# Performance work log

Measured on AMD Instinct MI355X. Metric: run time of the kernel, lower is better.

## Reference

```python
import jax, jax.numpy as jnp
import numpy as np

INF = 100000.0
B, W, T, U, S, N = 64, 16, 64, 128, 20, 8


def setup_inputs() -> dict:
    key = jax.random.key(0)
    ks = jax.random.split(key, 9)
    xavier = (2.0 / (U + U)) ** 0.5
    return {
        "slot_utt_h": jax.random.normal(ks[0], (B, W, T, U), jnp.float32),
        "slot_candidate_c": jax.random.normal(ks[1], (S, U), jnp.float32),
        "status_candidate_c": jax.random.normal(ks[2], (N, U), jnp.float32),
        "position_encoding": jax.random.normal(ks[3], (B, W, S, U), jnp.float32),
        "q_status": jax.random.normal(ks[4], (B, W, N, U), jnp.float32),
        "mask": jnp.zeros((B, W, S * N), jnp.float32),
        "weight": jax.random.normal(ks[5], (U, U), jnp.float32) * xavier,  # bilinear co-attention weight [U,U]
        "W1": jax.random.normal(ks[6], (2 * U, U), jnp.float32) * 0.05,
        "b1": jnp.zeros((U,), jnp.float32),
        "W2": jax.random.normal(ks[7], (U, U), jnp.float32) * 0.05,
        "b2": jnp.zeros((U,), jnp.float32),
        "W3": jax.random.normal(ks[8], (U, 1), jnp.float32) * 0.05,
        "b3": jnp.zeros((1,), jnp.float32),
    }


def _zero_mask(p):
    # original: -(p == 0).float() * INF, added before softmax
    return jnp.where(p == 0.0, -INF, 0.0)


def reference(slot_utt_h, slot_candidate_c, status_candidate_c, position_encoding,
              q_status, mask, weight, W1, b1, W2, b2, W3, b3):
    # ---- attention over utterance tokens ----
    # p[b,w,s,t] = <slot_candidate_c[s], slot_utt_h[b,w,t]>
    p = jnp.einsum('su,bwtu->bwst', slot_candidate_c, slot_utt_h)
    p = jax.nn.softmax(p + _zero_mask(p), axis=-1)
    q_slot = jnp.einsum('bwst,bwtu->bwsu', p, slot_utt_h) + position_encoding  # [B,W,S,U]

    # ---- bilinear co-attention: [B,W*S,U] @ weight @ [B,U,W*N] -> [B,W,S,W,N] ----
    co = jnp.einsum('bwsu,uv,bxnv->bwsxn', q_slot, weight, q_status)
    p2 = jax.nn.softmax(co + _zero_mask(co), axis=3)  # softmax over the second window axis x

    # weighted sum of statuses over window axis x
    q_status_slot = jnp.einsum('bwsxn,bxnu->bwsnu', p2, q_status)  # [B,W,S,N,U]

    q_slot_exp = jnp.broadcast_to(q_slot[:, :, :, None, :], (B, W, S, N, U))
    features = jnp.concatenate([q_slot_exp, q_status_slot], axis=-1)  # [B,W,S,N,2U]

    # ---- MLP (dropout in eval mode = identity) ----
    h = jax.nn.relu(features @ W1 + b1)
    h = jax.nn.relu(h @ W2 + b2)
    logits = h @ W3 + b3  # [B,W,S,N,1]

    logits = logits.reshape(B, W, S * N)
    slot_pred_logits = jnp.max(logits + mask, axis=1)  # masked max-pool over window
    slot_pred_labels = (slot_pred_logits > 0.0).astype(jnp.float32)
    return (slot_pred_labels, S * N, slot_pred_logits)
```

## Files before the change

### kernel.cpp

```cpp
#include <hip/hip_runtime.h>
#include <math.h>

#define INF_ 100000.0f
constexpr int B_ = 64, W_ = 16, T_ = 64, U_ = 128, S_ = 20, N_ = 8;

typedef unsigned short ushort_t;
typedef __attribute__((ext_vector_type(8))) short bf16x8;
typedef __attribute__((ext_vector_type(4))) float floatx4;

static __device__ __forceinline__ unsigned short f2bf(float x) {
    unsigned int u = __float_as_uint(x);
    return (unsigned short)((u + 0x7fff + ((u >> 16) & 1)) >> 16);
}
static __device__ __forceinline__ float bf2f(unsigned short s) {
    return __uint_as_float(((unsigned int)s) << 16);
}

#define HT_SWZ(u, t) ((u) * 72 + ((t) ^ ((((u) >> 3) & 7) << 3)))

__global__ __launch_bounds__(256) void kAP(
    const float* __restrict__ q_status, const float* __restrict__ weight,
    const float* __restrict__ W1, const float* __restrict__ W2,
    const float* __restrict__ c,
    const float* __restrict__ h,
    const float* __restrict__ pos,
    ushort_t* __restrict__ w1topT, ushort_t* __restrict__ w2T,
    ushort_t* __restrict__ Gt_bf, ushort_t* __restrict__ qs1T_bf,
    ushort_t* __restrict__ q_slot_bf)
{
    __shared__ __align__(16) ushort_t arena[17408];
    const int tid = threadIdx.x, bx = blockIdx.x;
    const int wave = tid >> 6, lane = tid & 63, m16 = lane & 15, q = lane >> 4;
    const bf16x8 zz = {0, 0, 0, 0, 0, 0, 0, 0};

    if (bx < 64) {
        const int b = bx;
        for (int i = tid * 4; i < 16384; i += 1024) {
            int r = i >> 7, v = i & 127;
            float4 wv = *(const float4*)&weight[i];
            *(ushort4*)&arena[r * 136 + v] =
                (ushort4){f2bf(wv.x), f2bf(wv.y), f2bf(wv.z), f2bf(wv.w)};
        }
        __syncthreads();
        const float* qb = q_status + (size_t)b * 16384;
        ushort_t* Gb = Gt_bf + (size_t)b * 16384;
#pragma unroll
        for (int mt2 = 0; mt2 < 2; ++mt2) {
            int mt = wave * 2 + mt2;
            int arow = mt * 16 + m16;
            bf16x8 afr[4];
#pragma unroll
            for (int kt = 0; kt < 4; ++kt) {
                const float* qp = &qb[arow * 128 + kt * 32 + q * 8];
                float4 c0 = *(const float4*)&qp[0];
                float4 c1 = *(const float4*)&qp[4];
                bf16x8 a;
                a[0] = (short)f2bf(c0.x); a[1] = (short)f2bf(c0.y);
                a[2] = (short)f2bf(c0.z); a[3] = (short)f2bf(c0.w);
                a[4] = (short)f2bf(c1.x); a[5] = (short)f2bf(c1.y);
                a[6] = (short)f2bf(c1.z); a[7] = (short)f2bf(c1.w);
                afr[kt] = a;
            }
#pragma unroll
            for (int jt = 0; jt < 8; ++jt) {
                floatx4 acc = {0.f, 0.f, 0.f, 0.f};
#pragma unroll
                for (int kt = 0; kt < 4; ++kt) {
                    bf16x8 w = *(const bf16x8*)&arena[(jt * 16 + m16) * 136 + kt * 32 + q * 8];
                    acc = __builtin_amdgcn_mfma_f32_16x16x32_bf16(afr[kt], w, acc, 0, 0, 0);
                }
#pragma unroll
                for (int reg = 0; reg < 4; ++reg)
                    Gb[(mt * 16 + q * 4 + reg) * 128 + jt * 16 + m16] = f2bf(acc[reg]);
            }
        }
        return;
    }
    if (bx < 128) {
        const int b = bx - 64;
        for (int i = tid * 4; i < 16384; i += 1024) {
            int v2 = i >> 7, j = i & 127;
            float4 wv = *(const float4*)&W1[(128 + v2) * 128 + j];
            arena[(j + 0) * 136 + v2] = f2bf(wv.x);
            arena[(j + 1) * 136 + v2] = f2bf(wv.y);
            arena[(j + 2) * 136 + v2] = f2bf(wv.z);
            arena[(j + 3) * 136 + v2] = f2bf(wv.w);
        }
        __syncthreads();
        const float* qb = q_status + (size_t)b * 16384;
        ushort_t* Qb = qs1T_bf + (size_t)b * 16384;
#pragma unroll
        for (int mt2 = 0; mt2 < 2; ++mt2) {
            int mt = wave * 2 + mt2;
            int arow = mt * 16 + m16;
            bf16x8 afr[4];
#pragma unroll
            for (int kt = 0; kt < 4; ++kt) {
                const float* qp = &qb[arow * 128 + kt * 32 + q * 8];
                float4 c0 = *(const float4*)&qp[0];
                float4 c1 = *(const float4*)&qp[4];
                bf16x8 a;
                a[0] = (short)f2bf(c0.x); a[1] = (short)f2bf(c0.y);
                a[2] = (short)f2bf(c0.z); a[3] = (short)f2bf(c0.w);
                a[4] = (short)f2bf(c1.x); a[5] = (short)f2bf(c1.y);
                a[6] = (short)f2bf(c1.z); a[7] = (short)f2bf(c1.w);
                afr[kt] = a;
            }
#pragma unroll
            for (int jt = 0; jt < 8; ++jt) {
                floatx4 acc = {0.f, 0.f, 0.f, 0.f};
#pragma unroll
                for (int kt = 0; kt < 4; ++kt) {
                    bf16x8 w = *(const bf16x8*)&arena[(jt * 16 + m16) * 136 + kt * 32 + q * 8];
                    acc = __builtin_amdgcn_mfma_f32_16x16x32_bf16(afr[kt], w, acc, 0, 0, 0);
                }
                ushort4 o = {f2bf(acc[0]), f2bf(acc[1]), f2bf(acc[2]), f2bf(acc[3])};
                *(ushort4*)&Qb[(jt * 16 + m16) * 128 + mt * 16 + q * 4] = o;
            }
        }
        return;
    }
    if (bx < 144) {
        int g = (bx - 128) * 1024 + tid * 4;
        int j = g >> 7, k = g & 127;
        *(ushort4*)&w1topT[g] =
            (ushort4){f2bf(W1[k * 128 + j]), f2bf(W1[(k + 1) * 128 + j]),
                      f2bf(W1[(k + 2) * 128 + j]), f2bf(W1[(k + 3) * 128 + j])};
        return;
    }
    if (bx < 160) {
        int g = (bx - 144) * 1024 + tid * 4;
        int j = g >> 7, k = g & 127;
        *(ushort4*)&w2T[g] =
            (ushort4){f2bf(W2[k * 128 + j]), f2bf(W2[(k + 1) * 128 + j]),
                      f2bf(W2[(k + 2) * 128 + j]), f2bf(W2[(k + 3) * 128 + j])};
        return;
    }

    ushort_t* sh_hT = arena;
    float*    sh_sc = (float*)(arena + 9216);
    ushort_t* sh_P  = arena + 13568;

    const int bw = bx - 160;
    const float* hb = h + (size_t)bw * 8192;

    for (int i = tid * 4; i < 8192; i += 1024) {
        int t = i >> 7, u = i & 127;
        float4 v = *(const float4*)&hb[i];
        sh_hT[HT_SWZ(u + 0, t)] = f2bf(v.x);
        sh_hT[HT_SWZ(u + 1, t)] = f2bf(v.y);
        sh_hT[HT_SWZ(u + 2, t)] = f2bf(v.z);
        sh_hT[HT_SWZ(u + 3, t)] = f2bf(v.w);
    }
    for (int i = tid; i < 2304; i += 256) sh_P[i] = 0;

#pragma unroll
    for (int ci = 0; ci < 2; ++ci) {
        int cmb = wave * 2 + ci;
        int mt = cmb >> 2, jt = cmb & 3;
        int arow = mt * 16 + m16;
        floatx4 acc = {0.f, 0.f, 0.f, 0.f};
#pragma unroll
        for (int kt = 0; kt < 4; ++kt) {
            bf16x8 a = zz;
            if (arow < 20) {
                const float* cp = &c[arow * 128 + kt * 32 + q * 8];
                float4 c0 = *(const float4*)&cp[0];
                float4 c1 = *(const float4*)&cp[4];
                a[0] = (short)f2bf(c0.x); a[1] = (short)f2bf(c0.y);
                a[2] = (short)f2bf(c0.z); a[3] = (short)f2bf(c0.w);
                a[4] = (short)f2bf(c1.x); a[5] = (short)f2bf(c1.y);
                a[6] = (short)f2bf(c1.z); a[7] = (short)f2bf(c1.w);
            }
            const float* hp = &hb[(jt * 16 + m16) * 128 + kt * 32 + q * 8];
            float4 b0 = *(const float4*)&hp[0];
            float4 b1v = *(const float4*)&hp[4];
            bf16x8 bb;
            bb[0] = (short)f2bf(b0.x); bb[1] = (short)f2bf(b0.y);
            bb[2] = (short)f2bf(b0.z); bb[3] = (short)f2bf(b0.w);
            bb[4] = (short)f2bf(b1v.x); bb[5] = (short)f2bf(b1v.y);
            bb[6] = (short)f2bf(b1v.z); bb[7] = (short)f2bf(b1v.w);
            acc = __builtin_amdgcn_mfma_f32_16x16x32_bf16(a, bb, acc, 0, 0, 0);
        }
#pragma unroll
        for (int reg = 0; reg < 4; ++reg)
            sh_sc[(mt * 16 + q * 4 + reg) * 68 + jt * 16 + m16] = acc[reg];
    }
    __syncthreads();

    for (int s = wave; s < 20; s += 4) {
        float v = sh_sc[s * 68 + lane];
        if (v == 0.0f) v = -INF_;
        float m = v;
        for (int d = 32; d; d >>= 1) m = fmaxf(m, __shfl_xor(m, d));
        float e = expf(v - m);
        float sum = e;
        for (int d = 32; d; d >>= 1) sum += __shfl_xor(sum, d);
        sh_P[s * 72 + lane] = f2bf(e / sum);
    }
    __syncthreads();

    const size_t obase = (size_t)bw * 2560;
#pragma unroll
    for (int ci = 0; ci < 4; ++ci) {
        int cmb = wave * 4 + ci;
        int mt = cmb >> 3, jt = cmb & 7;
        floatx4 acc = {0.f, 0.f, 0.f, 0.f};
#pragma unroll
        for (int kt = 0; kt < 2; ++kt) {
            bf16x8 a = *(const bf16x8*)&sh_P[(mt * 16 + m16) * 72 + kt * 32 + q * 8];
            bf16x8 b = *(const bf16x8*)&sh_hT[HT_SWZ(jt * 16 + m16, kt * 32 + q * 8)];
            acc = __builtin_amdgcn_mfma_f32_16x16x32_bf16(a, b, acc, 0, 0, 0);
        }
        int u = jt * 16 + m16;
#pragma unroll
        for (int reg = 0; reg < 4; ++reg) {
            int row = mt * 16 + q * 4 + reg;
            if (row < 20)
                q_slot_bf[obase + row * 128 + u] =
                    f2bf(acc[reg] + pos[obase + row * 128 + u]);
        }
    }
}

__global__ __launch_bounds__(640, 8) void kCp(
    const ushort_t* __restrict__ q_slot_bf,
    const ushort_t* __restrict__ Gt_bf,
    const ushort_t* __restrict__ w1topT,
    const float* __restrict__ b1,
    const ushort_t* __restrict__ qs1T_bf,
    const ushort_t* __restrict__ w2T,
    const float* __restrict__ b2,
    const float* __restrict__ W3,
    const float* __restrict__ b3,
    float* __restrict__ lg)
{
    __shared__ __align__(16) ushort_t arena[25328];
    float* Af = (float*)(arena + 20048);

    const int bw = blockIdx.x, b = bw >> 4, tid = threadIdx.x;
    const int wave = tid >> 6, lane = tid & 63, m16 = lane & 15, q = lane >> 4;
    const bf16x8 zz = {0, 0, 0, 0, 0, 0, 0, 0};

    for (int i = tid * 4; i < 16384; i += 2560) {
        int r = i >> 7, k = i & 127;
        *(ushort4*)&arena[r * 136 + k] = *(const ushort4*)&qs1T_bf[(size_t)b * 16384 + i];
    }
    {
        const ushort_t* qsl = q_slot_bf + (size_t)bw * 2560;
        const ushort_t* Gb = Gt_bf + (size_t)b * 16384;
        for (int t = wave; t < 32; t += 10) {
            int isA = t >> 4, tt = t & 15;
            int mt = tt >> 3, jt = tt & 7;
            int arow = mt * 16 + m16;
            const ushort_t* Bsrc = isA ? w1topT : Gb;
            floatx4 acc = {0.f, 0.f, 0.f, 0.f};
#pragma unroll
            for (int kt = 0; kt < 4; ++kt) {
                bf16x8 a = (arow < 20)
                    ? *(const bf16x8*)&qsl[arow * 128 + kt * 32 + q * 8] : zz;
                bf16x8 g = *(const bf16x8*)&Bsrc[(jt * 16 + m16) * 128 + kt * 32 + q * 8];
                acc = __builtin_amdgcn_mfma_f32_16x16x32_bf16(a, g, acc, 0, 0, 0);
            }
            int col = jt * 16 + m16;
            if (isA) {
                float bv = b1[col];
#pragma unroll
                for (int reg = 0; reg < 4; ++reg) {
                    int row = mt * 16 + q * 4 + reg;
                    if (row < 20) Af[row * 132 + col] = acc[reg] + bv;
                }
            } else {
#pragma unroll
                for (int reg = 0; reg < 4; ++reg) {
                    int row = mt * 16 + q * 4 + reg;
                    if (row < 20) arena[17408 + row * 132 + col] = f2bf(acc[reg]);
                }
            }
        }
    }
    __syncthreads();

    {
        int sn = tid >> 2, xi = tid & 3;
        int s = sn >> 3, n2 = sn & 7;
        const ushort_t* crow = &arena[17408 + s * 132];
        float v[4];
        float m = -INFINITY;
#pragma unroll
        for (int j = 0; j < 4; ++j) {
            float t = bf2f(crow[(xi + 4 * j) * 8 + n2]);
            if (t == 0.0f) t = -INF_;
            v[j] = t;
            m = fmaxf(m, t);
        }
        m = fmaxf(m, __shfl_xor(m, 1));
        m = fmaxf(m, __shfl_xor(m, 2));
        float sum = 0.f;
#pragma unroll
        for (int j = 0; j < 4; ++j) { v[j] = expf(v[j] - m); sum += v[j]; }
        sum += __shfl_xor(sum, 1);
        sum += __shfl_xor(sum, 2);
        float r = 1.0f / sum;
        __syncthreads();
#pragma unroll
        for (int j = 0; j < 4; ++j)
            arena[17408 + s * 132 + (xi + 4 * j) * 8 + n2] = f2bf(v[j] * r);
    }
    __syncthreads();

    const int n = m16 & 7;
    const int sIdx = wave * 2 + (m16 >> 3);

    floatx4 gacc[8];
#pragma unroll
    for (int mt = 0; mt < 8; ++mt) gacc[mt] = (floatx4){0.f, 0.f, 0.f, 0.f};
#pragma unroll
    for (int kt = 0; kt < 4; ++kt) {
        short pv = (short)arena[17408 + sIdx * 132 + kt * 32 + q * 8 + n];
        bf16x8 pf = {0, 0, 0, 0, 0, 0, 0, 0};
        pf[0] = (n == 0) ? pv : (short)0;
        pf[1] = (n == 1) ? pv : (short)0;
        pf[2] = (n == 2) ? pv : (short)0;
        pf[3] = (n == 3) ? pv : (short)0;
        pf[4] = (n == 4) ? pv : (short)0;
        pf[5] = (n == 5) ? pv : (short)0;
        pf[6] = (n == 6) ? pv : (short)0;
        pf[7] = (n == 7) ? pv : (short)0;
#pragma unroll
        for (int mt = 0; mt < 8; ++mt) {
            bf16x8 af = *(const bf16x8*)&arena[(mt * 16 + m16) * 136 + kt * 32 + q * 8];
            gacc[mt] = __builtin_amdgcn_mfma_f32_16x16x32_bf16(af, pf, gacc[mt], 0, 0, 0);
        }
    }

    unsigned int h1u[8][2];
    {
        const float* Ab = Af + sIdx * 132;
#pragma unroll
        for (int mt = 0; mt < 8; ++mt) {
            int u0 = mt * 16 + q * 4;
            float4 av = *(const float4*)&Ab[u0];
            unsigned int x0 = f2bf(fmaxf(gacc[mt][0] + av.x, 0.f));
            unsigned int x1 = f2bf(fmaxf(gacc[mt][1] + av.y, 0.f));
            unsigned int x2 = f2bf(fmaxf(gacc[mt][2] + av.z, 0.f));
            unsigned int x3 = f2bf(fmaxf(gacc[mt][3] + av.w, 0.f));
            h1u[mt][0] = x0 | (x1 << 16);
            h1u[mt][1] = x2 | (x3 << 16);
        }
    }
    __syncthreads();

    for (int i = tid * 4; i < 16384; i += 2560) {
        int r = i >> 7, k = i & 127;
        *(ushort4*)&arena[r * 136 + k] = *(const ushort4*)&w2T[i];
    }
    __syncthreads();

    floatx4 acc[8];
#pragma unroll
    for (int jt = 0; jt < 8; ++jt) acc[jt] = (floatx4){0.f, 0.f, 0.f, 0.f};

    const int sl0 = m16 + 16 * ((2 * q) & 3);
    const int sl1 = m16 + 16 * ((2 * q + 1) & 3);
    const bool hi = (q & 2);
#pragma unroll
    for (int kt = 0; kt < 4; ++kt) {
        int wa0 = __shfl((int)h1u[kt * 2 + 0][0], sl0);
        int wb0 = __shfl((int)h1u[kt * 2 + 1][0], sl0);
        int wa1 = __shfl((int)h1u[kt * 2 + 0][1], sl0);
        int wb1 = __shfl((int)h1u[kt * 2 + 1][1], sl0);
        int wa2 = __shfl((int)h1u[kt * 2 + 0][0], sl1);
        int wb2 = __shfl((int)h1u[kt * 2 + 1][0], sl1);
        int wa3 = __shfl((int)h1u[kt * 2 + 0][1], sl1);
        int wb3 = __shfl((int)h1u[kt * 2 + 1][1], sl1);
        int4 fr;
        fr.x = hi ? wb0 : wa0;
        fr.y = hi ? wb1 : wa1;
        fr.z = hi ? wb2 : wa2;
        fr.w = hi ? wb3 : wa3;
        bf16x8 af2 = *(bf16x8*)&fr;
        const int k0 = kt * 32 + q * 8;
#pragma unroll
        for (int jt = 0; jt < 8; ++jt) {
            bf16x8 bfr = *(const bf16x8*)&arena[(jt * 16 + m16) * 136 + k0];
            acc[jt] = __builtin_amdgcn_mfma_f32_16x16x32_bf16(af2, bfr, acc[jt], 0, 0, 0);
        }
    }

    float b2v[8], w3v[8];
#pragma unroll
    for (int jt = 0; jt < 8; ++jt) {
        b2v[jt] = b2[jt * 16 + m16];
        w3v[jt] = W3[jt * 16 + m16];
    }
    const float b3v = b3[0];
#pragma unroll
    for (int reg = 0; reg < 4; ++reg) {
        float p = 0.f;
#pragma unroll
        for (int jt = 0; jt < 8; ++jt)
            p += fmaxf(acc[jt][reg] + b2v[jt], 0.f) * w3v[jt];
        p += __shfl_xor(p, 1);
        p += __shfl_xor(p, 2);
        p += __shfl_xor(p, 4);
        p += __shfl_xor(p, 8);
        if (m16 == 0)
            lg[(size_t)bw * 160 + wave * 16 + q * 4 + reg] = p + b3v;
    }
}

__global__ __launch_bounds__(256) void k5_final(
    const float* __restrict__ lg,
    const float* __restrict__ mask,
    float* __restrict__ out)
{
    int idx = blockIdx.x * 256 + threadIdx.x;
    const int SN = S_ * N_;
    if (idx < B_ * SN) {
        int b = idx / SN, sn = idx % SN;
        float m = -INFINITY;
        for (int w = 0; w < W_; ++w) {
            float v = lg[((size_t)b * W_ + w) * SN + sn] + mask[((size_t)b * W_ + w) * SN + sn];
            m = fmaxf(m, v);
        }
        out[idx] = (m > 0.f) ? 1.f : 0.f;
        out[B_ * SN + 1 + idx] = m;
    }
    if (idx == 0) out[B_ * SN] = (float)SN;
}

extern "C" void kernel_launch(void* const* d_in, const int* in_sizes, int n_in,
                              void* d_out, int out_size, void* d_ws, size_t ws_size,
                              hipStream_t stream) {
    const float* slot_utt_h = (const float*)d_in[0];
    const float* slot_candidate_c = (const float*)d_in[1];
    const float* position_encoding = (const float*)d_in[3];
    const float* q_status = (const float*)d_in[4];
    const float* mask = (const float*)d_in[5];
    const float* weight = (const float*)d_in[6];
    const float* W1 = (const float*)d_in[7];
    const float* b1 = (const float*)d_in[8];
    const float* W2 = (const float*)d_in[9];
    const float* b2 = (const float*)d_in[10];
    const float* W3 = (const float*)d_in[11];
    const float* b3 = (const float*)d_in[12];
    float* out = (float*)d_out;

    float* f = (float*)d_ws;
    float*    lg        = f + 0;
    ushort_t* q_slot_bf = (ushort_t*)(f + 163840);
    ushort_t* Gt_bf     = (ushort_t*)(f + 1474560);
    ushort_t* qs1T_bf   = (ushort_t*)(f + 1998848);
    ushort_t* w1topT    = (ushort_t*)(f + 2523136);
    ushort_t* w2T       = (ushort_t*)(f + 2531328);

    kAP<<<1184, 256, 0, stream>>>(q_status, weight, W1, W2,
                                  slot_candidate_c, slot_utt_h,
                                  position_encoding,
                                  w1topT, w2T, Gt_bf, qs1T_bf, q_slot_bf);
    kCp<<<1024, 640, 0, stream>>>(q_slot_bf, Gt_bf, w1topT, b1, qs1T_bf,
                                  w2T, b2, W3, b3, lg);
    k5_final<<<(B_ * S_ * N_ + 255) / 256, 256, 0, stream>>>(lg, mask, out);
}
```

Baseline: 186.2 us.

## Split co-attention and W1 projection GEMMs into a separate batched kernel

Moves the q_slot x G co-attention product and the q_slot x W1top projection out of the per-(b,w) kernel into a new kernel. That kernel stages the B operand in shared memory and computes 64-row tiles across windows, so each block reuses G or W1top far more than the old 20-row blocks, which read B straight from global memory. The results (co in bf16, A in fp32) now round-trip through global workspace, adding an extra launch and extra memory traffic, and the remaining kernel's occupancy hint changes from 8 to 5.

```diff
diff --git a/kernel.cpp b/kernel.cpp
--- a/kernel.cpp
+++ b/kernel.cpp
@@ -223,68 +223,99 @@
     }
 }
 
-__global__ __launch_bounds__(640, 8) void kCp(
+__global__ __launch_bounds__(256) void kB(
     const ushort_t* __restrict__ q_slot_bf,
     const ushort_t* __restrict__ Gt_bf,
     const ushort_t* __restrict__ w1topT,
     const float* __restrict__ b1,
+    ushort_t* __restrict__ co_bf,
+    float* __restrict__ A)
+{
+    __shared__ __align__(16) ushort_t shB[128 * 136];
+    const int tid = threadIdx.x, bx = blockIdx.x;
+    const int wave = tid >> 6, lane = tid & 63, m16 = lane & 15, q = lane >> 4;
+
+    if (bx < 320) {
+        const int b = bx / 5, rt = bx - b * 5;
+        for (int i = tid * 4; i < 16384; i += 1024)
+            *(ushort4*)&shB[(i >> 7) * 136 + (i & 127)] =
+                *(const ushort4*)&Gt_bf[(size_t)b * 16384 + i];
+        __syncthreads();
+
+        const size_t rbase = (size_t)b * 320 + rt * 64 + wave * 16;
+        floatx4 acc[8];
+#pragma unroll
+        for (int jt = 0; jt < 8; ++jt) acc[jt] = (floatx4){0.f, 0.f, 0.f, 0.f};
+#pragma unroll
+        for (int kt = 0; kt < 4; ++kt) {
+            bf16x8 a = *(const bf16x8*)&q_slot_bf[(rbase + m16) * 128 + kt * 32 + q * 8];
+#pragma unroll
+            for (int jt = 0; jt < 8; ++jt) {
+                bf16x8 g = *(const bf16x8*)&shB[(jt * 16 + m16) * 136 + kt * 32 + q * 8];
+                acc[jt] = __builtin_amdgcn_mfma_f32_16x16x32_bf16(a, g, acc[jt], 0, 0, 0);
+            }
+        }
+#pragma unroll
+        for (int jt = 0; jt < 8; ++jt)
+#pragma unroll
+            for (int reg = 0; reg < 4; ++reg)
+                co_bf[(rbase + q * 4 + reg) * 128 + jt * 16 + m16] = f2bf(acc[jt][reg]);
+    } else {
+        const int blk = bx - 320;
+        for (int i = tid * 4; i < 16384; i += 1024)
+            *(ushort4*)&shB[(i >> 7) * 136 + (i & 127)] =
+                *(const ushort4*)&w1topT[i];
+        __syncthreads();
+
+        const size_t rbase = (size_t)blk * 64 + wave * 16;
+        floatx4 acc[8];
+#pragma unroll
+        for (int jt = 0; jt < 8; ++jt) acc[jt] = (floatx4){0.f, 0.f, 0.f, 0.f};
+#pragma unroll
+        for (int kt = 0; kt < 4; ++kt) {
+            bf16x8 a = *(const bf16x8*)&q_slot_bf[(rbase + m16) * 128 + kt * 32 + q * 8];
+#pragma unroll
+            for (int jt = 0; jt < 8; ++jt) {
+                bf16x8 g = *(const bf16x8*)&shB[(jt * 16 + m16) * 136 + kt * 32 + q * 8];
+                acc[jt] = __builtin_amdgcn_mfma_f32_16x16x32_bf16(a, g, acc[jt], 0, 0, 0);
+            }
+        }
+#pragma unroll
+        for (int jt = 0; jt < 8; ++jt) {
+            int col = jt * 16 + m16;
+            float bv = b1[col];
+#pragma unroll
+            for (int reg = 0; reg < 4; ++reg)
+                A[(rbase + q * 4 + reg) * 128 + col] = acc[jt][reg] + bv;
+        }
+    }
+}
+
+__global__ __launch_bounds__(640, 5) void kC(
+    const ushort_t* __restrict__ co_bf,
     const ushort_t* __restrict__ qs1T_bf,
+    const float* __restrict__ A,
     const ushort_t* __restrict__ w2T,
     const float* __restrict__ b2,
     const float* __restrict__ W3,
     const float* __restrict__ b3,
     float* __restrict__ lg)
 {
-    __shared__ __align__(16) ushort_t arena[25328];
-    float* Af = (float*)(arena + 20048);
+    __shared__ __align__(16) ushort_t shB[128 * 136];
+    __shared__ __align__(16) ushort_t shP[20 * 132];
 
     const int bw = blockIdx.x, b = bw >> 4, tid = threadIdx.x;
     const int wave = tid >> 6, lane = tid & 63, m16 = lane & 15, q = lane >> 4;
-    const bf16x8 zz = {0, 0, 0, 0, 0, 0, 0, 0};
 
     for (int i = tid * 4; i < 16384; i += 2560) {
         int r = i >> 7, k = i & 127;
-        *(ushort4*)&arena[r * 136 + k] = *(const ushort4*)&qs1T_bf[(size_t)b * 16384 + i];
-    }
-    {
-        const ushort_t* qsl = q_slot_bf + (size_t)bw * 2560;
-        const ushort_t* Gb = Gt_bf + (size_t)b * 16384;
-        for (int t = wave; t < 32; t += 10) {
-            int isA = t >> 4, tt = t & 15;
-            int mt = tt >> 3, jt = tt & 7;
-            int arow = mt * 16 + m16;
-            const ushort_t* Bsrc = isA ? w1topT : Gb;
-            floatx4 acc = {0.f, 0.f, 0.f, 0.f};
-#pragma unroll
-            for (int kt = 0; kt < 4; ++kt) {
-                bf16x8 a = (arow < 20)
-                    ? *(const bf16x8*)&qsl[arow * 128 + kt * 32 + q * 8] : zz;
-                bf16x8 g = *(const bf16x8*)&Bsrc[(jt * 16 + m16) * 128 + kt * 32 + q * 8];
-                acc = __builtin_amdgcn_mfma_f32_16x16x32_bf16(a, g, acc, 0, 0, 0);
-            }
-            int col = jt * 16 + m16;
-            if (isA) {
-                float bv = b1[col];
-#pragma unroll
-                for (int reg = 0; reg < 4; ++reg) {
-                    int row = mt * 16 + q * 4 + reg;
-                    if (row < 20) Af[row * 132 + col] = acc[reg] + bv;
-                }
-            } else {
-#pragma unroll
-                for (int reg = 0; reg < 4; ++reg) {
-                    int row = mt * 16 + q * 4 + reg;
-                    if (row < 20) arena[17408 + row * 132 + col] = f2bf(acc[reg]);
-                }
-            }
-        }
-    }
-    __syncthreads();
+        *(ushort4*)&shB[r * 136 + k] = *(const ushort4*)&qs1T_bf[(size_t)b * 16384 + i];
+    }
 
     {
         int sn = tid >> 2, xi = tid & 3;
         int s = sn >> 3, n2 = sn & 7;
-        const ushort_t* crow = &arena[17408 + s * 132];
+        const ushort_t* crow = co_bf + ((size_t)bw * 20 + s) * 128;
         float v[4];
         float m = -INFINITY;
 #pragma unroll
@@ -302,10 +333,9 @@
         sum += __shfl_xor(sum, 1);
         sum += __shfl_xor(sum, 2);
         float r = 1.0f / sum;
-        __syncthreads();
 #pragma unroll
         for (int j = 0; j < 4; ++j)
-            arena[17408 + s * 132 + (xi + 4 * j) * 8 + n2] = f2bf(v[j] * r);
+            shP[s * 132 + (xi + 4 * j) * 8 + n2] = f2bf(v[j] * r);
     }
     __syncthreads();
 
@@ -317,7 +347,7 @@
     for (int mt = 0; mt < 8; ++mt) gacc[mt] = (floatx4){0.f, 0.f, 0.f, 0.f};
 #pragma unroll
     for (int kt = 0; kt < 4; ++kt) {
-        short pv = (short)arena[17408 + sIdx * 132 + kt * 32 + q * 8 + n];
+        short pv = (short)shP[sIdx * 132 + kt * 32 + q * 8 + n];
         bf16x8 pf = {0, 0, 0, 0, 0, 0, 0, 0};
         pf[0] = (n == 0) ? pv : (short)0;
         pf[1] = (n == 1) ? pv : (short)0;
@@ -329,14 +359,14 @@
         pf[7] = (n == 7) ? pv : (short)0;
 #pragma unroll
         for (int mt = 0; mt < 8; ++mt) {
-            bf16x8 af = *(const bf16x8*)&arena[(mt * 16 + m16) * 136 + kt * 32 + q * 8];
+            bf16x8 af = *(const bf16x8*)&shB[(mt * 16 + m16) * 136 + kt * 32 + q * 8];
             gacc[mt] = __builtin_amdgcn_mfma_f32_16x16x32_bf16(af, pf, gacc[mt], 0, 0, 0);
         }
     }
 
     unsigned int h1u[8][2];
     {
-        const float* Ab = Af + sIdx * 132;
+        const float* Ab = A + ((size_t)bw * 20 + sIdx) * 128;
 #pragma unroll
         for (int mt = 0; mt < 8; ++mt) {
             int u0 = mt * 16 + q * 4;
@@ -353,7 +383,7 @@
 
     for (int i = tid * 4; i < 16384; i += 2560) {
         int r = i >> 7, k = i & 127;
-        *(ushort4*)&arena[r * 136 + k] = *(const ushort4*)&w2T[i];
+        *(ushort4*)&shB[r * 136 + k] = *(const ushort4*)&w2T[i];
     }
     __syncthreads();
 
@@ -383,7 +413,7 @@
         const int k0 = kt * 32 + q * 8;
 #pragma unroll
         for (int jt = 0; jt < 8; ++jt) {
-            bf16x8 bfr = *(const bf16x8*)&arena[(jt * 16 + m16) * 136 + k0];
+            bf16x8 bfr = *(const bf16x8*)&shB[(jt * 16 + m16) * 136 + k0];
             acc[jt] = __builtin_amdgcn_mfma_f32_16x16x32_bf16(af2, bfr, acc[jt], 0, 0, 0);
         }
     }
@@ -449,17 +479,19 @@
 
     float* f = (float*)d_ws;
     float*    lg        = f + 0;
-    ushort_t* q_slot_bf = (ushort_t*)(f + 163840);
-    ushort_t* Gt_bf     = (ushort_t*)(f + 1474560);
-    ushort_t* qs1T_bf   = (ushort_t*)(f + 1998848);
-    ushort_t* w1topT    = (ushort_t*)(f + 2523136);
-    ushort_t* w2T       = (ushort_t*)(f + 2531328);
+    float*    A         = f + 163840;
+    ushort_t* q_slot_bf = (ushort_t*)(f + 2785280);
+    ushort_t* co_bf     = (ushort_t*)(f + 4096000);
+    ushort_t* Gt_bf     = (ushort_t*)(f + 5406720);
+    ushort_t* qs1T_bf   = (ushort_t*)(f + 5931008);
+    ushort_t* w1topT    = (ushort_t*)(f + 6455296);
+    ushort_t* w2T       = (ushort_t*)(f + 6463488);
 
     kAP<<<1184, 256, 0, stream>>>(q_status, weight, W1, W2,
                                   slot_candidate_c, slot_utt_h,
                                   position_encoding,
                                   w1topT, w2T, Gt_bf, qs1T_bf, q_slot_bf);
-    kCp<<<1024, 640, 0, stream>>>(q_slot_bf, Gt_bf, w1topT, b1, qs1T_bf,
-                                  w2T, b2, W3, b3, lg);
+    kB<<<640, 256, 0, stream>>>(q_slot_bf, Gt_bf, w1topT, b1, co_bf, A);
+    kC<<<1024, 640, 0, stream>>>(co_bf, qs1T_bf, A, w2T, b2, W3, b3, lg);
     k5_final<<<(B_ * S_ * N_ + 255) / 256, 256, 0, stream>>>(lg, mask, out);
 }
```

Measured after the change: 181.8 us. 2.4% less time.
